# Kernel optimization log

Measured on AMD Instinct MI355X. Metric: run time of the kernel, lower is better.

The kernel has to match this reference:

```python
import jax, jax.numpy as jnp
import numpy as np

B, SEQ, ST, DIN, DK, DV = 2, 4096, 128, 1024, 64, 64
T = SEQ + 2 * ST  # 4352, divisible by 8 -> no pad branch in original


def _l2norm(t):
    # matches torch F.normalize(p=2, dim=-1, eps=1e-12)
    return t / jnp.maximum(jnp.linalg.norm(t, axis=-1, keepdims=True), 1e-12)


def setup_inputs() -> dict:
    key = jax.random.key(0)
    ks = jax.random.split(key, 9)
    x = jax.random.normal(ks[0], (B, T, DIN), dtype=jnp.float32)
    w = 0.02
    Wq = jax.random.normal(ks[1], (DK, DIN), dtype=jnp.float32) * w
    Wk = jax.random.normal(ks[2], (DK, DIN), dtype=jnp.float32) * w
    Wv = jax.random.normal(ks[3], (DV, DIN), dtype=jnp.float32) * w
    Wq_s = jax.random.normal(ks[4], (DK, DIN), dtype=jnp.float32) * w
    Wk_s = jax.random.normal(ks[5], (DK, DIN), dtype=jnp.float32) * w
    Wv_s = jax.random.normal(ks[6], (DV, DIN), dtype=jnp.float32) * w
    cope_emb = jax.random.normal(ks[7], (DK, T), dtype=jnp.float32)  # (1, dim_key, seq_len+2*state_len) squeezed
    scale = jnp.array([0.125], dtype=jnp.float32)  # learnable scaling_factor param
    return {"x": x, "Wq": Wq, "Wk": Wk, "Wv": Wv, "Wq_s": Wq_s,
            "Wk_s": Wk_s, "Wv_s": Wv_s, "cope_emb": cope_emb, "scale": scale}


def reference(x, Wq, Wk, Wv, Wq_s, Wk_s, Wv_s, cope_emb, scale):
    # extract_state: start-state, sequence, end-state
    xs, xm, xe = x[:, :ST], x[:, ST:ST + SEQ], x[:, ST + SEQ:]
    # project (Linear, no bias) then L2-normalize each token vector
    q = jnp.concatenate([_l2norm(xs @ Wq_s.T), _l2norm(xm @ Wq.T), _l2norm(xe @ Wq_s.T)], axis=1)
    k = jnp.concatenate([_l2norm(xs @ Wk_s.T), _l2norm(xm @ Wk.T), _l2norm(xe @ Wk_s.T)], axis=1)
    v = jnp.concatenate([_l2norm(xs @ Wv_s.T), _l2norm(xm @ Wv.T), _l2norm(xe @ Wv_s.T)], axis=1)

    # q@k^T is used both for CoPE gates and (scaled) attention scores
    logits = jnp.einsum('btd,bsd->bts', q, k)  # (B, T, T)

    # --- CoPE bias ---
    gates = jax.nn.sigmoid(logits)
    pos = jnp.cumsum(gates[:, :, ::-1], axis=-1)[:, :, ::-1]  # flip-cumsum-flip
    pos = jnp.minimum(pos, jnp.float32(T - 1))
    pos_floor = jnp.floor(pos)
    pos_ceil = jnp.ceil(pos)
    w = pos - pos_floor
    logits_int = jnp.einsum('btd,dl->btl', q, cope_emb)  # (B, T, T)
    lc = jnp.take_along_axis(logits_int, pos_ceil.astype(jnp.int32), axis=-1)
    lf = jnp.take_along_axis(logits_int, pos_floor.astype(jnp.int32), axis=-1)
    cope_bias = lc * w + lf * (1.0 - w)

    # --- causal + state-token mask: tril, with end-state rows blocked from start-state cols ---
    i = jnp.arange(T)
    mask = i[:, None] >= i[None, :]
    blocked = (i[:, None] >= SEQ + ST) & (i[None, :] < ST)
    mask = mask & (~blocked)
    attn_bias = jnp.where(mask, 0.0, -jnp.inf)[None, :, :]

    scores = logits * scale[0] + attn_bias + cope_bias
    att = jax.nn.softmax(scores, axis=-1) @ v  # (B, T, DV)
    return att
```

## Files before the change

### kernel.cpp

```cpp
#include <hip/hip_runtime.h>
#include <math.h>

#define B_ 2
#define SEQ_ 4096
#define ST_ 128
#define T_ 4352
#define DIN_ 1024
#define NW 16
#define LMAX 3328
#define LPAD 3336
#define NSLICE 272
#define NROW 8704

typedef _Float16 f16;
typedef __attribute__((ext_vector_type(8))) _Float16 f16x8;
typedef __attribute__((ext_vector_type(4))) float f32x4;

#define OB_WH  0
#define OB_WL  786432
#define OB_QH  1572864
#define OB_QL  2686976
#define OB_KH  3801088
#define OB_KL  4915200
#define OB_VT  6029312
#define OB_CPT 7143424
#define OB_SS  7569408
#define OB_XH  17039360
#define OB_XL  34865152
#define NEED_NEW 52690944ull

#define WT4_OFF 0
#define Q_OFF   393216
#define KT_OFF  950272
#define V_OFF   1507328

__device__ __forceinline__ int wuid() {
  return __builtin_amdgcn_readfirstlane((int)(threadIdx.x >> 6));
}

template<int CTRL, int RM>
__device__ __forceinline__ float dppadd(float x) {
  int y = __builtin_amdgcn_update_dpp(0, __float_as_int(x), CTRL, RM, 0xf, true);
  return x + __int_as_float(y);
}
__device__ __forceinline__ float wave_iscan(float x) {
  x = dppadd<0x111, 0xf>(x);
  x = dppadd<0x112, 0xf>(x);
  x = dppadd<0x114, 0xf>(x);
  x = dppadd<0x118, 0xf>(x);
  x = dppadd<0x142, 0xa>(x);
  x = dppadd<0x143, 0xc>(x);
  return x;
}
__device__ __forceinline__ float p16scan(float x) {
  x = dppadd<0x111, 0xf>(x);
  x = dppadd<0x112, 0xf>(x);
  x = dppadd<0x114, 0xf>(x);
  x = dppadd<0x118, 0xf>(x);
  return x;
}
__device__ __forceinline__ float swz15(float x) {
  return __int_as_float(__builtin_amdgcn_ds_swizzle(__float_as_int(x), 0x1F0));
}

__global__ __launch_bounds__(256) void wsplit_kernel(
    const float* __restrict__ Wq,  const float* __restrict__ Wk,
    const float* __restrict__ Wv,  const float* __restrict__ Wqs,
    const float* __restrict__ Wks, const float* __restrict__ Wvs,
    f16* __restrict__ wh, f16* __restrict__ wl) {
  const int m = blockIdx.y;
  const float* src = (m==0)?Wq:(m==1)?Wqs:(m==2)?Wk:(m==3)?Wks:(m==4)?Wv:Wvs;
  const int g0 = (int)blockIdx.x * 4096 + (int)threadIdx.x * 16;
  const float4* s4 = reinterpret_cast<const float4*>(src + g0);
  float4 v0 = s4[0], v1 = s4[1], v2 = s4[2], v3 = s4[3];
  f16x8 h0, h1, l0, l1;
  h0[0]=(f16)v0.x; h0[1]=(f16)v0.y; h0[2]=(f16)v0.z; h0[3]=(f16)v0.w;
  h0[4]=(f16)v1.x; h0[5]=(f16)v1.y; h0[6]=(f16)v1.z; h0[7]=(f16)v1.w;
  h1[0]=(f16)v2.x; h1[1]=(f16)v2.y; h1[2]=(f16)v2.z; h1[3]=(f16)v2.w;
  h1[4]=(f16)v3.x; h1[5]=(f16)v3.y; h1[6]=(f16)v3.z; h1[7]=(f16)v3.w;
  l0[0]=(f16)(v0.x-(float)h0[0]); l0[1]=(f16)(v0.y-(float)h0[1]);
  l0[2]=(f16)(v0.z-(float)h0[2]); l0[3]=(f16)(v0.w-(float)h0[3]);
  l0[4]=(f16)(v1.x-(float)h0[4]); l0[5]=(f16)(v1.y-(float)h0[5]);
  l0[6]=(f16)(v1.z-(float)h0[6]); l0[7]=(f16)(v1.w-(float)h0[7]);
  l1[0]=(f16)(v2.x-(float)h1[0]); l1[1]=(f16)(v2.y-(float)h1[1]);
  l1[2]=(f16)(v2.z-(float)h1[2]); l1[3]=(f16)(v2.w-(float)h1[3]);
  l1[4]=(f16)(v3.x-(float)h1[4]); l1[5]=(f16)(v3.y-(float)h1[5]);
  l1[6]=(f16)(v3.z-(float)h1[6]); l1[7]=(f16)(v3.w-(float)h1[7]);
  const size_t o = (size_t)m * 65536 + g0;
  *reinterpret_cast<f16x8*>(wh + o) = h0;
  *reinterpret_cast<f16x8*>(wh + o + 8) = h1;
  *reinterpret_cast<f16x8*>(wl + o) = l0;
  *reinterpret_cast<f16x8*>(wl + o + 8) = l1;
}

__global__ __launch_bounds__(256) void xsplit_kernel(
    const float* __restrict__ x, f16* __restrict__ xh, f16* __restrict__ xl) {
  const size_t g0 = ((size_t)blockIdx.x * 256 + threadIdx.x) * 16;
  const float4* s4 = reinterpret_cast<const float4*>(x + g0);
  float4 v0 = s4[0], v1 = s4[1], v2 = s4[2], v3 = s4[3];
  f16x8 h0, h1, l0, l1;
  h0[0]=(f16)v0.x; h0[1]=(f16)v0.y; h0[2]=(f16)v0.z; h0[3]=(f16)v0.w;
  h0[4]=(f16)v1.x; h0[5]=(f16)v1.y; h0[6]=(f16)v1.z; h0[7]=(f16)v1.w;
  h1[0]=(f16)v2.x; h1[1]=(f16)v2.y; h1[2]=(f16)v2.z; h1[3]=(f16)v2.w;
  h1[4]=(f16)v3.x; h1[5]=(f16)v3.y; h1[6]=(f16)v3.z; h1[7]=(f16)v3.w;
  l0[0]=(f16)(v0.x-(float)h0[0]); l0[1]=(f16)(v0.y-(float)h0[1]);
  l0[2]=(f16)(v0.z-(float)h0[2]); l0[3]=(f16)(v0.w-(float)h0[3]);
  l0[4]=(f16)(v1.x-(float)h0[4]); l0[5]=(f16)(v1.y-(float)h0[5]);
  l0[6]=(f16)(v1.z-(float)h0[6]); l0[7]=(f16)(v1.w-(float)h0[7]);
  l1[0]=(f16)(v2.x-(float)h1[0]); l1[1]=(f16)(v2.y-(float)h1[1]);
  l1[2]=(f16)(v2.z-(float)h1[2]); l1[3]=(f16)(v2.w-(float)h1[3]);
  l1[4]=(f16)(v3.x-(float)h1[4]); l1[5]=(f16)(v3.y-(float)h1[5]);
  l1[6]=(f16)(v3.z-(float)h1[6]); l1[7]=(f16)(v3.w-(float)h1[7]);
  *reinterpret_cast<f16x8*>(xh + g0) = h0;
  *reinterpret_cast<f16x8*>(xh + g0 + 8) = h1;
  *reinterpret_cast<f16x8*>(xl + g0) = l0;
  *reinterpret_cast<f16x8*>(xl + g0 + 8) = l1;
}

__global__ __launch_bounds__(256) void copet_kernel(
    const float* __restrict__ cope, f16* __restrict__ copeT) {
  __shared__ float t2[64][65];
  const int l0 = blockIdx.x << 6;
  const int tid = (int)threadIdx.x;
  #pragma unroll
  for (int p = 0; p < 16; ++p) {
    int d = (p << 2) + (tid >> 6), c = tid & 63;
    t2[d][c] = cope[(size_t)d * T_ + l0 + c];
  }
  __syncthreads();
  #pragma unroll
  for (int p = 0; p < 16; ++p) {
    int l = (p << 2) + (tid >> 6), d = tid & 63;
    copeT[(size_t)(l0 + l) * 64 + d] = (f16)t2[d][l];
  }
}

#define PM_MFMA(ACC, WHP, WLP) { \
  f16x8 bh_ = *reinterpret_cast<const f16x8*>((WHP) + (st << 5)); \
  f16x8 bl_ = *reinterpret_cast<const f16x8*>((WLP) + (st << 5)); \
  ACC = __builtin_amdgcn_mfma_f32_16x16x32_f16(xh_, bh_, ACC, 0, 0, 0); \
  ACC = __builtin_amdgcn_mfma_f32_16x16x32_f16(xl_, bh_, ACC, 0, 0, 0); \
  ACC = __builtin_amdgcn_mfma_f32_16x16x32_f16(xh_, bl_, ACC, 0, 0, 0); }

#define PM_RED(ACC, P) { \
  float s0_ = ACC[0]*ACC[0], s1_ = ACC[1]*ACC[1], s2_ = ACC[2]*ACC[2], s3_ = ACC[3]*ACC[3]; \
  s0_ += __shfl_xor(s0_, 1, 64); s1_ += __shfl_xor(s1_, 1, 64); \
  s2_ += __shfl_xor(s2_, 1, 64); s3_ += __shfl_xor(s3_, 1, 64); \
  s0_ += __shfl_xor(s0_, 2, 64); s1_ += __shfl_xor(s1_, 2, 64); \
  s2_ += __shfl_xor(s2_, 2, 64); s3_ += __shfl_xor(s3_, 2, 64); \
  s0_ += __shfl_xor(s0_, 4, 64); s1_ += __shfl_xor(s1_, 4, 64); \
  s2_ += __shfl_xor(s2_, 4, 64); s3_ += __shfl_xor(s3_, 4, 64); \
  s0_ += __shfl_xor(s0_, 8, 64); s1_ += __shfl_xor(s1_, 8, 64); \
  s2_ += __shfl_xor(s2_, 8, 64); s3_ += __shfl_xor(s3_, 8, 64); \
  if (qlo == 0) { \
    ssq[wn][P][(qhi << 2) + 0] = s0_; ssq[wn][P][(qhi << 2) + 1] = s1_; \
    ssq[wn][P][(qhi << 2) + 2] = s2_; ssq[wn][P][(qhi << 2) + 3] = s3_; } }

#define PM_QK1(ACC, P, HH, LL, RG) { \
  float tt_ = ssq[0][P][(qhi << 2) + RG] + ssq[1][P][(qhi << 2) + RG] \
            + ssq[2][P][(qhi << 2) + RG] + ssq[3][P][(qhi << 2) + RG]; \
  float rn_ = 1.f / fmaxf(sqrtf(tt_), 1e-12f); \
  float v_ = ACC[RG] * rn_; \
  f16 h_ = (f16)v_; \
  size_t ad_ = (size_t)(bt0 + (qhi << 2) + RG) * 64 + (wn << 4) + qlo; \
  HH[ad_] = h_; LL[ad_] = (f16)(v_ - (float)h_); }

#define PM_V1(ACC, P, RG) { \
  float tt_ = ssq[0][P][(qhi << 2) + RG] + ssq[1][P][(qhi << 2) + RG] \
            + ssq[2][P][(qhi << 2) + RG] + ssq[3][P][(qhi << 2) + RG]; \
  float rn_ = 1.f / fmaxf(sqrtf(tt_), 1e-12f); \
  vt[(size_t)(b * 64 + (wn << 4) + qlo) * T_ + t0 + (qhi << 2) + RG] = (f16)(ACC[RG] * rn_); }

__global__ __launch_bounds__(512, 4) void projM_kernel(
    const f16* __restrict__ xh, const f16* __restrict__ xl,
    const f16* __restrict__ wh, const f16* __restrict__ wl,
    f16* __restrict__ qh, f16* __restrict__ ql,
    f16* __restrict__ kh, f16* __restrict__ kl,
    f16* __restrict__ vt) {
  __shared__ float ssq[4][3][16];
  __shared__ float part[4][64][12];
  const int lane = (int)threadIdx.x & 63;
  const int w = wuid();
  const int wn = w & 3;
  const int kh2 = w >> 2;
  const int qlo = lane & 15, qhi = lane >> 4;
  const int bt0 = (int)blockIdx.x << 4;
  const int b = bt0 / T_;
  const int t0 = bt0 - b * T_;
  const int spec = (t0 < ST_ || t0 >= ST_ + SEQ_) ? 1 : 0;

  const int kof = kh2 << 9;
  const f16* xhr = xh + (size_t)(bt0 + qlo) * DIN_ + kof + (qhi << 3);
  const f16* xlr = xl + (size_t)(bt0 + qlo) * DIN_ + kof + (qhi << 3);
  const size_t wrow = (size_t)((wn << 4) + qlo) * 1024 + kof + (qhi << 3);
  const f16* wq  = wh + (size_t)(0 + spec) * 65536 + wrow;
  const f16* wqL = wl + (size_t)(0 + spec) * 65536 + wrow;
  const f16* wk  = wh + (size_t)(2 + spec) * 65536 + wrow;
  const f16* wkL = wl + (size_t)(2 + spec) * 65536 + wrow;
  const f16* wv  = wh + (size_t)(4 + spec) * 65536 + wrow;
  const f16* wvL = wl + (size_t)(4 + spec) * 65536 + wrow;

  f32x4 aq = {0.f,0.f,0.f,0.f}, ak = {0.f,0.f,0.f,0.f}, av = {0.f,0.f,0.f,0.f};

  #pragma unroll 4
  for (int st = 0; st < 16; ++st) {
    f16x8 xh_ = *reinterpret_cast<const f16x8*>(xhr + (st << 5));
    f16x8 xl_ = *reinterpret_cast<const f16x8*>(xlr + (st << 5));
    PM_MFMA(aq, wq, wqL)
    PM_MFMA(ak, wk, wkL)
    PM_MFMA(av, wv, wvL)
  }

  if (w >= 4) {
    float* p = &part[w - 4][lane][0];
    p[0] = aq[0]; p[1] = aq[1]; p[2]  = aq[2]; p[3]  = aq[3];
    p[4] = ak[0]; p[5] = ak[1]; p[6]  = ak[2]; p[7]  = ak[3];
    p[8] = av[0]; p[9] = av[1]; p[10] = av[2]; p[11] = av[3];
  }
  __syncthreads();
  if (w < 4) {
    const float* p = &part[w][lane][0];
    aq[0] += p[0]; aq[1] += p[1]; aq[2] += p[2];  aq[3] += p[3];
    ak[0] += p[4]; ak[1] += p[5]; ak[2] += p[6];  ak[3] += p[7];
    av[0] += p[8]; av[1] += p[9]; av[2] += p[10]; av[3] += p[11];
    PM_RED(aq, 0) PM_RED(ak, 1) PM_RED(av, 2)
  }
  __syncthreads();
  if (w < 4) {
    PM_QK1(aq, 0, qh, ql, 0) PM_QK1(aq, 0, qh, ql, 1)
    PM_QK1(aq, 0, qh, ql, 2) PM_QK1(aq, 0, qh, ql, 3)
    PM_QK1(ak, 1, kh, kl, 0) PM_QK1(ak, 1, kh, kl, 1)
    PM_QK1(ak, 1, kh, kl, 2) PM_QK1(ak, 1, kh, kl, 3)
    PM_V1(av, 2, 0) PM_V1(av, 2, 1) PM_V1(av, 2, 2) PM_V1(av, 2, 3)
  }
}

__global__ __launch_bounds__(512, 4) void gscan_kernel(
    const f16* __restrict__ qh, const f16* __restrict__ kh,
    float* __restrict__ ss) {
  __shared__ float sl[16][NSLICE];
  const int lane = (int)threadIdx.x & 63;
  const int w = wuid();
  const int qlo = lane & 15, qhi = lane >> 4;
  const int rowg0 = (int)blockIdx.x << 4;
  const int b = rowg0 / T_;
  const size_t bT64 = (size_t)(b * T_) * 64;
  const f16* qrp = qh + (size_t)(rowg0 + qlo) * 64 + (qhi << 3);
  f16x8 aqh0 = *reinterpret_cast<const f16x8*>(qrp);
  f16x8 aqh1 = *reinterpret_cast<const f16x8*>(qrp + 32);

  for (int i = 0; i < 34; ++i) {
    const int sli = w * 34 + i;
    const int sg = (sli << 4) + qlo;
    const f16* krh_ = kh + bT64 + (size_t)sg * 64 + (qhi << 3);
    f16x8 bh0 = *reinterpret_cast<const f16x8*>(krh_);
    f16x8 bh1 = *reinterpret_cast<const f16x8*>(krh_ + 32);
    f32x4 a = {0.f, 0.f, 0.f, 0.f};
    a = __builtin_amdgcn_mfma_f32_16x16x32_f16(aqh0, bh0, a, 0, 0, 0);
    a = __builtin_amdgcn_mfma_f32_16x16x32_f16(aqh1, bh1, a, 0, 0, 0);
    float g0 = 1.f / (1.f + __expf(-a[0])); float s0 = p16scan(g0);
    float g1 = 1.f / (1.f + __expf(-a[1])); float s1 = p16scan(g1);
    float g2 = 1.f / (1.f + __expf(-a[2])); float s2 = p16scan(g2);
    float g3 = 1.f / (1.f + __expf(-a[3])); float s3 = p16scan(g3);
    if (qlo == 15) {
      sl[(qhi << 2) + 0][sli] = s0;
      sl[(qhi << 2) + 1][sli] = s1;
      sl[(qhi << 2) + 2][sli] = s2;
      sl[(qhi << 2) + 3][sli] = s3;
    }
  }
  __syncthreads();
  #pragma unroll
  for (int rr = 0; rr < 2; ++rr) {
    const int row = (w << 1) | rr;
    const float* r = &sl[row][0];
    const int base = NSLICE - 1 - 5 * lane;
    double v0 = 0.0, v1 = 0.0, v2 = 0.0, v3 = 0.0, v4 = 0.0;
    double acc = 0.0;
    if (base - 0 >= 0) { acc += (double)r[base - 0]; } v0 = acc;
    if (base - 1 >= 0) { acc += (double)r[base - 1]; } v1 = acc;
    if (base - 2 >= 0) { acc += (double)r[base - 2]; } v2 = acc;
    if (base - 3 >= 0) { acc += (double)r[base - 3]; } v3 = acc;
    if (base - 4 >= 0) { acc += (double)r[base - 4]; } v4 = acc;
    double x = acc;
    #pragma unroll
    for (int off = 1; off < 64; off <<= 1) {
      double y = __shfl_up(x, off, 64);
      if (lane >= off) x += y;
    }
    const double offn = x - acc;
    float* go = ss + (size_t)(rowg0 + row) * NSLICE;
    if (base - 0 >= 0) go[base - 0] = (float)(v0 + offn);
    if (base - 1 >= 0) go[base - 1] = (float)(v1 + offn);
    if (base - 2 >= 0) go[base - 2] = (float)(v2 + offn);
    if (base - 3 >= 0) go[base - 3] = (float)(v3 + offn);
    if (base - 4 >= 0) go[base - 4] = (float)(v4 + offn);
  }
}

#define QKD(SF, NF) { \
  int sg_ = swb + (NF << 4) + qlo; \
  int scl_ = sg_ < T_ ? sg_ : T_ - 1; \
  const f16* krh_ = kh + bT64 + (size_t)scl_ * 64 + (qhi << 3); \
  f16x8 bh0_ = *reinterpret_cast<const f16x8*>(krh_); \
  f16x8 bh1_ = *reinterpret_cast<const f16x8*>(krh_ + 32); \
  f32x4 a_ = {0.f, 0.f, 0.f, 0.f}; \
  a_ = __builtin_amdgcn_mfma_f32_16x16x32_f16(aqh0, bh0_, a_, 0, 0, 0); \
  a_ = __builtin_amdgcn_mfma_f32_16x16x32_f16(aqh1, bh1_, a_, 0, 0, 0); \
  SF = a_; }

#define PXA(SF, RG, SSV, LF, LC, WF) { \
  float g_ = 1.f / (1.f + __expf(-SF[RG])); \
  float in_ = p16scan(g_); \
  float pos_ = SSV - in_ + g_; \
  pos_ = pos_ < 0.f ? 0.f : (pos_ > 3326.f ? 3326.f : pos_); \
  int idx_ = (int)pos_; \
  WF = pos_ - (float)idx_; \
  const f16* lrow_ = liL + ((qhi << 2) + RG) * LPAD + idx_; \
  LF = (float)lrow_[0]; LC = (float)lrow_[1]; }

#define PXB(SF, NF, RG, LF, LC, WF) { \
  int sg_ = swb + (NF << 4) + qlo; \
  float bias_ = fmaf(WF, LC - LF, LF); \
  int tl_ = t0 + (qhi << 2) + RG; \
  bool valid_ = (sg_ <= tl_) && !((tl_ >= ST_ + SEQ_) && (sg_ < ST_)); \
  float p_ = valid_ ? __expf(fmaf(SF[RG], sc, bias_) - mrw[RG]) : 0.f; \
  lsum[RG] += p_; \
  pst[((qhi << 2) + RG) * 40 + (NF << 4) + qlo] = (f16)p_; }

#define PVF(OA, NF) { \
  int d_ = (NF << 4) + qlo; \
  const f16* vr_ = vt + (size_t)(b * 64 + d_) * T_; \
  f16x8 v0_ = *reinterpret_cast<const f16x8*>(vr_ + sv0); \
  OA = __builtin_amdgcn_mfma_f32_16x16x32_f16(pa0, v0_, OA, 0, 0, 0); }

#define OST(OA, NF) { \
  ob[w * 1024 + ((qhi << 2) + 0) * 64 + (NF << 4) + qlo] = OA[0]; \
  ob[w * 1024 + ((qhi << 2) + 1) * 64 + (NF << 4) + qlo] = OA[1]; \
  ob[w * 1024 + ((qhi << 2) + 2) * 64 + (NF << 4) + qlo] = OA[2]; \
  ob[w * 1024 + ((qhi << 2) + 3) * 64 + (NF << 4) + qlo] = OA[3]; }

__global__ __launch_bounds__(1024, 4) void attnD_kernel(
    const f16* __restrict__ qh, const f16* __restrict__ kh,
    const f16* __restrict__ vt, const f16* __restrict__ cpt,
    const float* __restrict__ ss,
    const float* __restrict__ scalep, float* __restrict__ out) {
  __shared__ __align__(16) f16 liL[16 * LPAD];
  __shared__ __align__(16) f16 pstage[NW * 16 * 40];
  __shared__ float totF[NW][16];
  __shared__ float rmxS[NW][16];

  const int tid = (int)threadIdx.x;
  const int lane = tid & 63;
  const int w = wuid();
  const int bt0 = ((int)(gridDim.x - 1 - blockIdx.x)) << 4;
  const int b = bt0 / T_;
  const int t0 = bt0 - b * T_;
  const float sc = scalep[0];
  const int qlo = lane & 15, qhi = lane >> 4;

  const f16* qrp = qh + (size_t)(bt0 + qlo) * 64 + (qhi << 3);
  f16x8 aqh0 = *reinterpret_cast<const f16x8*>(qrp);
  f16x8 aqh1 = *reinterpret_cast<const f16x8*>(qrp + 32);

  {
    f32x4 rm = {-1e30f, -1e30f, -1e30f, -1e30f};
    #pragma unroll 2
    for (int c = 0; c < 13; ++c) {
      const int lf = w * 208 + (c << 4);
      const f16* cr = cpt + (size_t)(lf + qlo) * 64 + (qhi << 3);
      f16x8 b0 = *reinterpret_cast<const f16x8*>(cr);
      f16x8 b1 = *reinterpret_cast<const f16x8*>(cr + 32);
      f32x4 a = {0.f, 0.f, 0.f, 0.f};
      a = __builtin_amdgcn_mfma_f32_16x16x32_f16(aqh0, b0, a, 0, 0, 0);
      a = __builtin_amdgcn_mfma_f32_16x16x32_f16(aqh1, b1, a, 0, 0, 0);
      f16 h0_ = (f16)a[0]; liL[((qhi << 2) + 0) * LPAD + lf + qlo] = h0_; rm[0] = fmaxf(rm[0], (float)h0_);
      f16 h1_ = (f16)a[1]; liL[((qhi << 2) + 1) * LPAD + lf + qlo] = h1_; rm[1] = fmaxf(rm[1], (float)h1_);
      f16 h2_ = (f16)a[2]; liL[((qhi << 2) + 2) * LPAD + lf + qlo] = h2_; rm[2] = fmaxf(rm[2], (float)h2_);
      f16 h3_ = (f16)a[3]; liL[((qhi << 2) + 3) * LPAD + lf + qlo] = h3_; rm[3] = fmaxf(rm[3], (float)h3_);
    }
    #pragma unroll
    for (int k = 1; k < 16; k <<= 1) {
      rm[0] = fmaxf(rm[0], __shfl_xor(rm[0], k, 64));
      rm[1] = fmaxf(rm[1], __shfl_xor(rm[1], k, 64));
      rm[2] = fmaxf(rm[2], __shfl_xor(rm[2], k, 64));
      rm[3] = fmaxf(rm[3], __shfl_xor(rm[3], k, 64));
    }
    if (qlo == 0) {
      rmxS[w][(qhi << 2) + 0] = rm[0];
      rmxS[w][(qhi << 2) + 1] = rm[1];
      rmxS[w][(qhi << 2) + 2] = rm[2];
      rmxS[w][(qhi << 2) + 3] = rm[3];
    }
  }
  __syncthreads();
  f32x4 mrw;
  #pragma unroll
  for (int reg = 0; reg < 4; ++reg) {
    float mm = rmxS[0][(qhi << 2) + reg];
    #pragma unroll
    for (int w2 = 1; w2 < NW; ++w2) mm = fmaxf(mm, rmxS[w2][(qhi << 2) + reg]);
    mrw[reg] = mm + fabsf(sc) + 2e-3f;
  }

  f16* pst = pstage + w * 640;
  const size_t bT64 = (size_t)(b * T_) * 64;
  const float* ssl = ss + (size_t)(bt0 + (qhi << 2)) * NSLICE;

  f32x4 o0 = {0.f,0.f,0.f,0.f}, o1 = {0.f,0.f,0.f,0.f};
  f32x4 o2 = {0.f,0.f,0.f,0.f}, o3 = {0.f,0.f,0.f,0.f};
  f32x4 lsum = {0.f,0.f,0.f,0.f};

  const int jtmax = (t0 + 15) >> 9;
  for (int jt = jtmax; jt >= 0; --jt) {
    const int swb = (jt << 9) + (w << 5);
    f32x4 sf0, sf1;
    QKD(sf0, 0) QKD(sf1, 1)
    const int sbr = swb >> 4;
    const int sb0 = sbr < (NSLICE - 1) ? sbr : (NSLICE - 1);
    const int sb1 = (sbr + 1) < (NSLICE - 1) ? (sbr + 1) : (NSLICE - 1);
    float sA0 = ssl[0 * NSLICE + sb0];
    float sA1 = ssl[1 * NSLICE + sb0];
    float sA2 = ssl[2 * NSLICE + sb0];
    float sA3 = ssl[3 * NSLICE + sb0];
    float sB0 = ssl[0 * NSLICE + sb1];
    float sB1 = ssl[1 * NSLICE + sb1];
    float sB2 = ssl[2 * NSLICE + sb1];
    float sB3 = ssl[3 * NSLICE + sb1];
    float lf0, lc0, wf0, lf1, lc1, wf1, lf2, lc2, wf2, lf3, lc3, wf3;
    float lf4, lc4, wf4, lf5, lc5, wf5, lf6, lc6, wf6, lf7, lc7, wf7;
    PXA(sf0, 0, sA0, lf0, lc0, wf0) PXA(sf0, 1, sA1, lf1, lc1, wf1)
    PXA(sf0, 2, sA2, lf2, lc2, wf2) PXA(sf0, 3, sA3, lf3, lc3, wf3)
    PXA(sf1, 0, sB0, lf4, lc4, wf4) PXA(sf1, 1, sB1, lf5, lc5, wf5)
    PXA(sf1, 2, sB2, lf6, lc6, wf6) PXA(sf1, 3, sB3, lf7, lc7, wf7)
    PXB(sf0, 0, 0, lf0, lc0, wf0) PXB(sf0, 0, 1, lf1, lc1, wf1)
    PXB(sf0, 0, 2, lf2, lc2, wf2) PXB(sf0, 0, 3, lf3, lc3, wf3)
    PXB(sf1, 1, 0, lf4, lc4, wf4) PXB(sf1, 1, 1, lf5, lc5, wf5)
    PXB(sf1, 1, 2, lf6, lc6, wf6) PXB(sf1, 1, 3, lf7, lc7, wf7)
    {
      const f16* pr = pst + qlo * 40;
      f16x8 pa0 = *reinterpret_cast<const f16x8*>(pr + (qhi << 3));
      int sv0 = swb + (qhi << 3);
      sv0 = sv0 < T_ - 8 ? sv0 : T_ - 8;
      PVF(o0, 0) PVF(o1, 1) PVF(o2, 2) PVF(o3, 3)
    }
  }

  #pragma unroll
  for (int k = 1; k < 16; k <<= 1) {
    lsum[0] += __shfl_xor(lsum[0], k, 64);
    lsum[1] += __shfl_xor(lsum[1], k, 64);
    lsum[2] += __shfl_xor(lsum[2], k, 64);
    lsum[3] += __shfl_xor(lsum[3], k, 64);
  }
  __syncthreads();
  if (qlo == 0) {
    totF[w][(qhi << 2) + 0] = lsum[0];
    totF[w][(qhi << 2) + 1] = lsum[1];
    totF[w][(qhi << 2) + 2] = lsum[2];
    totF[w][(qhi << 2) + 3] = lsum[3];
  }
  float* ob = reinterpret_cast<float*>(liL);
  OST(o0, 0) OST(o1, 1) OST(o2, 2) OST(o3, 3)
  __syncthreads();
  {
    const int r = tid >> 6, d = tid & 63;
    float L = 0.f, o = 0.f;
    #pragma unroll
    for (int w2 = 0; w2 < NW; ++w2) {
      L += totF[w2][r];
      o += ob[w2 * 1024 + tid];
    }
    out[(size_t)(bt0 + r) * 64 + d] = o / L;
  }
}

__global__ __launch_bounds__(256) void wtrans_kernel(
    const float* __restrict__ Wq,  const float* __restrict__ Wk,
    const float* __restrict__ Wv,  const float* __restrict__ Wqs,
    const float* __restrict__ Wks, const float* __restrict__ Wvs,
    float* __restrict__ ws) {
  const int m = blockIdx.y;
  const float* src = (m==0)?Wq:(m==1)?Wqs:(m==2)?Wk:(m==3)?Wks:(m==4)?Wv:Wvs;
  float* dst = ws + (size_t)m * (DIN_*64);
  const int bx = blockIdx.x;
  #pragma unroll
  for (int p = 0; p < 16; ++p) {
    int e = (int)threadIdx.x + (p << 8);
    int c = e & 3, o = (e >> 2) & 63;
    int i = (bx << 6) + (p << 2) + c;
    dst[(((bx << 4) + p) * 64 + o) * 4 + c] = src[o * DIN_ + i];
  }
}

__global__ __launch_bounds__(256) void proj_kernel(
    const float* __restrict__ x, float* __restrict__ ws) {
  __shared__ float tile[32][65];
  const int t0 = blockIdx.x << 5;
  const int b  = blockIdx.y;
  const int pj = blockIdx.z;
  const int spec = (t0 < ST_ || t0 >= ST_ + SEQ_) ? 1 : 0;
  const float4* W4 = reinterpret_cast<const float4*>(ws + WT4_OFF + (size_t)(pj*2 + spec) * (DIN_*64));
  const int lane = (int)threadIdx.x & 63;
  const int w = wuid();
  const float* xb = x + ((size_t)(b * T_ + t0 + (w << 3))) * DIN_;
  float acc[8] = {0.f,0.f,0.f,0.f,0.f,0.f,0.f,0.f};
  #pragma unroll 4
  for (int i4 = 0; i4 < 256; ++i4) {
    float4 wv = W4[(i4 << 6) + lane];
    #pragma unroll
    for (int r = 0; r < 8; ++r) {
      float4 xv = reinterpret_cast<const float4*>(xb + r * DIN_)[i4];
      acc[r] = fmaf(wv.x, xv.x, fmaf(wv.y, xv.y, fmaf(wv.z, xv.z, fmaf(wv.w, xv.w, acc[r]))));
    }
  }
  float outv[8];
  #pragma unroll
  for (int r = 0; r < 8; ++r) {
    float sq = acc[r] * acc[r];
    #pragma unroll
    for (int off = 32; off; off >>= 1) sq += __shfl_xor(sq, off, 64);
    float n = fmaxf(sqrtf(sq), 1e-12f);
    outv[r] = acc[r] / n;
  }
  const int trow = t0 + (w << 3);
  if (pj != 1) {
    float* dst = ws + (pj == 0 ? Q_OFF : V_OFF) + ((size_t)(b * T_ + trow)) * 64;
    #pragma unroll
    for (int r = 0; r < 8; ++r) dst[r * 64 + lane] = outv[r];
  } else {
    #pragma unroll
    for (int r = 0; r < 8; ++r) tile[(w << 3) + r][lane] = outv[r];
    __syncthreads();
    float* kt = ws + KT_OFF + (size_t)b * 16 * T_ * 4;
    #pragma unroll
    for (int p = 0; p < 8; ++p) {
      int e = (int)threadIdx.x + (p << 8);
      int c = e & 3, tt = (e >> 2) & 31, d4 = e >> 7;
      kt[((size_t)d4 * T_ + t0 + tt) * 4 + c] = tile[tt][(d4 << 2) + c];
    }
  }
}

__global__ __launch_bounds__(1024) void attn_kernel(
    const float* __restrict__ ws_c, const float* __restrict__ cope,
    const float* __restrict__ scalep, float* __restrict__ out) {
  __shared__ float li_s[8 * T_];
  __shared__ float pbuf[NW][8][32];
  __shared__ float totF[NW][8];
  __shared__ double suffD[NW][8];
  __shared__ double carryD[2][8];
  __shared__ float mlL[NW][8];
  __shared__ float wmax[NW][8];
  const int tid = (int)threadIdx.x;
  const int lane = tid & 63;
  const int w = wuid();
  const int t0 = ((int)(gridDim.x - 1 - blockIdx.x)) << 3;
  const int b  = blockIdx.y;
  const float* qrow = ws_c + Q_OFF + ((size_t)(b * T_ + t0)) * 64;
  const float* ktb  = ws_c + KT_OFF + (size_t)b * 16 * T_ * 4;
  const float* vb   = ws_c + V_OFF + ((size_t)b * T_) * 64;
  const float sc = scalep[0];
  if (tid < 8) carryD[0][tid] = 0.0;
  float lm[8];
  #pragma unroll
  for (int r = 0; r < 8; ++r) lm[r] = -INFINITY;
  for (int jt = 0; jt < 5; ++jt) {
    const int l = (jt << 10) + tid;
    if (l < T_) {
      float a[8] = {0,0,0,0,0,0,0,0};
      #pragma unroll 4
      for (int d4 = 0; d4 < 16; ++d4) {
        float c0 = cope[(d4 * 4 + 0) * T_ + l];
        float c1 = cope[(d4 * 4 + 1) * T_ + l];
        float c2 = cope[(d4 * 4 + 2) * T_ + l];
        float c3 = cope[(d4 * 4 + 3) * T_ + l];
        #pragma unroll
        for (int r = 0; r < 8; ++r) {
          float4 qq = *reinterpret_cast<const float4*>(qrow + r * 64 + (d4 << 2));
          a[r] = fmaf(c0, qq.x, fmaf(c1, qq.y, fmaf(c2, qq.z, fmaf(c3, qq.w, a[r]))));
        }
      }
      #pragma unroll
      for (int r = 0; r < 8; ++r) { li_s[r * T_ + l] = a[r]; lm[r] = fmaxf(lm[r], a[r]); }
    }
  }
  #pragma unroll
  for (int r = 0; r < 8; ++r) {
    #pragma unroll
    for (int off = 32; off; off >>= 1) lm[r] = fmaxf(lm[r], __shfl_xor(lm[r], off, 64));
  }
  if (lane == 0) {
    #pragma unroll
    for (int r = 0; r < 8; ++r) wmax[w][r] = lm[r];
  }
  __syncthreads();
  float mrow[8];
  #pragma unroll
  for (int r = 0; r < 8; ++r) {
    float mm = wmax[0][r];
    #pragma unroll
    for (int w2 = 1; w2 < NW; ++w2) mm = fmaxf(mm, wmax[w2][r]);
    mrow[r] = mm + fabsf(sc) + 1e-3f;
  }
  float acc[8]  = {0,0,0,0,0,0,0,0};
  float lsum[8] = {0,0,0,0,0,0,0,0};
  int par = 0;
  for (int jt = 4; jt >= 0; --jt) {
    const int s = (jt << 10) + tid;
    const bool sval = (s < T_);
    float lg[8] = {0,0,0,0,0,0,0,0};
    if (sval) {
      #pragma unroll 4
      for (int d4 = 0; d4 < 16; ++d4) {
        float4 kk = *reinterpret_cast<const float4*>(ktb + ((size_t)d4 * T_ + s) * 4);
        #pragma unroll
        for (int r = 0; r < 8; ++r) {
          float4 qq = *reinterpret_cast<const float4*>(qrow + r * 64 + (d4 << 2));
          lg[r] = fmaf(kk.x, qq.x, fmaf(kk.y, qq.y, fmaf(kk.z, qq.z, fmaf(kk.w, qq.w, lg[r]))));
        }
      }
    }
    float locsuf[8], gtot[8];
    #pragma unroll
    for (int r = 0; r < 8; ++r) {
      float g = sval ? 1.f / (1.f + __expf(-lg[r])) : 0.f;
      float xx = wave_iscan(g);
      float tt = __shfl(xx, 63, 64);
      locsuf[r] = tt - xx + g;
      gtot[r] = tt;
    }
    if (lane == 0) {
      #pragma unroll
      for (int r = 0; r < 8; ++r) totF[w][r] = gtot[r];
    }
    __syncthreads();
    if (tid < 128) {
      const int w2 = tid >> 3, r = tid & 7;
      float ssum = 0.f;
      for (int w3 = w2 + 1; w3 < NW; ++w3) ssum += totF[w3][r];
      suffD[w2][r] = carryD[par][r] + (double)ssum;
      if (w2 == 0) carryD[par ^ 1][r] = carryD[par][r] + (double)(ssum + totF[0][r]);
    }
    __syncthreads();
    par ^= 1;
    if ((jt << 10) > t0 + 7) continue;
    float p[8];
    #pragma unroll
    for (int r = 0; r < 8; ++r) {
      double posd = suffD[w][r] + (double)locsuf[r];
      if (posd > 4351.0) posd = 4351.0;
      int idx = (int)posd;
      float wf = (float)(posd - (double)idx);
      int idx2 = idx < 4351 ? idx + 1 : 4351;
      float lf = li_s[r * T_ + idx];
      float lc = li_s[r * T_ + idx2];
      float bias = fmaf(wf, lc - lf, lf);
      const int t = t0 + r;
      const bool valid = sval && (s <= t) && !((t >= ST_ + SEQ_) && (s < ST_));
      float score = valid ? fmaf(lg[r], sc, bias) : -INFINITY;
      p[r] = __expf(score - mrow[r]);
      lsum[r] += p[r];
    }
    const int sbase = (jt << 10) + (w << 6);
    if (sbase < T_) {
      #pragma unroll
      for (int pass = 0; pass < 2; ++pass) {
        if ((lane >> 5) == pass) {
          #pragma unroll
          for (int r = 0; r < 8; ++r) pbuf[w][r][lane & 31] = p[r];
        }
        const int s0 = sbase + (pass << 5);
        #pragma unroll 4
        for (int s4 = 0; s4 < 8; ++s4) {
          const int sb = s0 + (s4 << 2);
          float v0 = vb[(size_t)(sb + 0) * 64 + lane];
          float v1 = vb[(size_t)(sb + 1) * 64 + lane];
          float v2 = vb[(size_t)(sb + 2) * 64 + lane];
          float v3 = vb[(size_t)(sb + 3) * 64 + lane];
          #pragma unroll
          for (int r = 0; r < 8; ++r) {
            float4 pr = *reinterpret_cast<const float4*>(&pbuf[w][r][s4 << 2]);
            acc[r] = fmaf(pr.x, v0, fmaf(pr.y, v1, fmaf(pr.z, v2, fmaf(pr.w, v3, acc[r]))));
          }
        }
      }
    }
  }
  #pragma unroll
  for (int r = 0; r < 8; ++r) {
    #pragma unroll
    for (int off = 32; off; off >>= 1) lsum[r] += __shfl_xor(lsum[r], off, 64);
  }
  if (lane == 0) {
    #pragma unroll
    for (int r = 0; r < 8; ++r) mlL[w][r] = lsum[r];
  }
  float* pb = &pbuf[w][0][0];
  #pragma unroll
  for (int pass = 0; pass < 2; ++pass) {
    __syncthreads();
    #pragma unroll
    for (int rr = 0; rr < 4; ++rr) pb[rr * 64 + lane] = acc[pass * 4 + rr];
    __syncthreads();
    if (tid < 256) {
      const int rr = tid >> 6, d = tid & 63;
      const int r = pass * 4 + rr;
      float o = 0.f, L = 0.f;
      #pragma unroll
      for (int w2 = 0; w2 < NW; ++w2) {
        o += (&pbuf[w2][0][0])[rr * 64 + d];
        L += mlL[w2][r];
      }
      out[((size_t)(b * T_ + t0 + r)) * 64 + d] = o / L;
    }
  }
}

extern "C" void kernel_launch(void* const* d_in, const int* in_sizes, int n_in,
                              void* d_out, int out_size, void* d_ws, size_t ws_size,
                              hipStream_t stream) {
  const float* x    = (const float*)d_in[0];
  const float* Wq   = (const float*)d_in[1];
  const float* Wk   = (const float*)d_in[2];
  const float* Wv   = (const float*)d_in[3];
  const float* Wqs  = (const float*)d_in[4];
  const float* Wks  = (const float*)d_in[5];
  const float* Wvs  = (const float*)d_in[6];
  const float* cope = (const float*)d_in[7];
  const float* scl  = (const float*)d_in[8];
  float* outp = (float*)d_out;
  (void)in_sizes; (void)n_in; (void)out_size;

  if (ws_size >= NEED_NEW) {
    unsigned char* wb = (unsigned char*)d_ws;
    f16* whp = (f16*)(wb + OB_WH);
    f16* wlp = (f16*)(wb + OB_WL);
    f16* qh = (f16*)(wb + OB_QH);
    f16* ql = (f16*)(wb + OB_QL);
    f16* kh = (f16*)(wb + OB_KH);
    f16* kl = (f16*)(wb + OB_KL);
    f16* vt = (f16*)(wb + OB_VT);
    f16* cpt = (f16*)(wb + OB_CPT);
    float* ssp = (float*)(wb + OB_SS);
    f16* xhp = (f16*)(wb + OB_XH);
    f16* xlp = (f16*)(wb + OB_XL);
    hipLaunchKernelGGL(wsplit_kernel, dim3(16, 6), dim3(256), 0, stream,
                       Wq, Wk, Wv, Wqs, Wks, Wvs, whp, wlp);
    hipLaunchKernelGGL(xsplit_kernel, dim3(2176), dim3(256), 0, stream, x, xhp, xlp);
    hipLaunchKernelGGL(copet_kernel, dim3(52), dim3(256), 0, stream, cope, cpt);
    hipLaunchKernelGGL(projM_kernel, dim3(544), dim3(512), 0, stream,
                       xhp, xlp, whp, wlp, qh, ql, kh, kl, vt);
    hipLaunchKernelGGL(gscan_kernel, dim3(544), dim3(512), 0, stream, qh, kh, ssp);
    hipLaunchKernelGGL(attnD_kernel, dim3(544), dim3(1024), 0, stream,
                       qh, kh, vt, cpt, ssp, scl, outp);
  } else {
    float* ws = (float*)d_ws;
    hipLaunchKernelGGL(wtrans_kernel, dim3(16, 6), dim3(256), 0, stream,
                       Wq, Wk, Wv, Wqs, Wks, Wvs, ws);
    hipLaunchKernelGGL(proj_kernel, dim3(136, 2, 3), dim3(256), 0, stream, x, ws);
    hipLaunchKernelGGL(attn_kernel, dim3(544, 2), dim3(1024), 0, stream, ws, cope, scl, outp);
  }
}
```

Baseline: 251.9 us.

## Fuse gate suffix-scan kernel into attention kernel via shared-memory slice sums

Merges the separate gscan kernel into the attention kernel. Each block now computes the per-slice sigmoid-gate sums and their reverse prefix scan itself, keeps them in shared memory, and reads them from there instead of from a global buffer. This removes a kernel launch and the global write and read of the slice-sum array. In exchange each attention block does the full-row QK gate scan inline, adding shared memory and work to a kernel that is already heavy, which may reduce occupancy.

After: 250.5 us. About the same (-0.5%).

```diff
diff --git a/kernel.cpp b/kernel.cpp
--- a/kernel.cpp
+++ b/kernel.cpp
@@ -235,22 +235,105 @@
   }
 }
 
-__global__ __launch_bounds__(512, 4) void gscan_kernel(
+#define QKD(SF, NF) { \
+  int sg_ = swb + (NF << 4) + qlo; \
+  int scl_ = sg_ < T_ ? sg_ : T_ - 1; \
+  const f16* krh_ = kh + bT64 + (size_t)scl_ * 64 + (qhi << 3); \
+  f16x8 bh0_ = *reinterpret_cast<const f16x8*>(krh_); \
+  f16x8 bh1_ = *reinterpret_cast<const f16x8*>(krh_ + 32); \
+  f32x4 a_ = {0.f, 0.f, 0.f, 0.f}; \
+  a_ = __builtin_amdgcn_mfma_f32_16x16x32_f16(aqh0, bh0_, a_, 0, 0, 0); \
+  a_ = __builtin_amdgcn_mfma_f32_16x16x32_f16(aqh1, bh1_, a_, 0, 0, 0); \
+  SF = a_; }
+
+#define PXA(SF, RG, SSV, LF, LC, WF) { \
+  float g_ = 1.f / (1.f + __expf(-SF[RG])); \
+  float in_ = p16scan(g_); \
+  float pos_ = SSV - in_ + g_; \
+  pos_ = pos_ < 0.f ? 0.f : (pos_ > 3326.f ? 3326.f : pos_); \
+  int idx_ = (int)pos_; \
+  WF = pos_ - (float)idx_; \
+  const f16* lrow_ = liL + ((qhi << 2) + RG) * LPAD + idx_; \
+  LF = (float)lrow_[0]; LC = (float)lrow_[1]; }
+
+#define PXB(SF, NF, RG, LF, LC, WF) { \
+  int sg_ = swb + (NF << 4) + qlo; \
+  float bias_ = fmaf(WF, LC - LF, LF); \
+  int tl_ = t0 + (qhi << 2) + RG; \
+  bool valid_ = (sg_ <= tl_) && !((tl_ >= ST_ + SEQ_) && (sg_ < ST_)); \
+  float p_ = valid_ ? __expf(fmaf(SF[RG], sc, bias_) - mrw[RG]) : 0.f; \
+  lsum[RG] += p_; \
+  pst[((qhi << 2) + RG) * 40 + (NF << 4) + qlo] = (f16)p_; }
+
+#define PVF(OA, NF) { \
+  int d_ = (NF << 4) + qlo; \
+  const f16* vr_ = vt + (size_t)(b * 64 + d_) * T_; \
+  f16x8 v0_ = *reinterpret_cast<const f16x8*>(vr_ + sv0); \
+  OA = __builtin_amdgcn_mfma_f32_16x16x32_f16(pa0, v0_, OA, 0, 0, 0); }
+
+#define OST(OA, NF) { \
+  ob[w * 1024 + ((qhi << 2) + 0) * 64 + (NF << 4) + qlo] = OA[0]; \
+  ob[w * 1024 + ((qhi << 2) + 1) * 64 + (NF << 4) + qlo] = OA[1]; \
+  ob[w * 1024 + ((qhi << 2) + 2) * 64 + (NF << 4) + qlo] = OA[2]; \
+  ob[w * 1024 + ((qhi << 2) + 3) * 64 + (NF << 4) + qlo] = OA[3]; }
+
+__global__ __launch_bounds__(1024, 4) void attnE_kernel(
     const f16* __restrict__ qh, const f16* __restrict__ kh,
-    float* __restrict__ ss) {
+    const f16* __restrict__ vt, const f16* __restrict__ cpt,
+    const float* __restrict__ scalep, float* __restrict__ out) {
+  __shared__ __align__(16) f16 liL[16 * LPAD];
+  __shared__ __align__(16) f16 pstage[NW * 16 * 40];
   __shared__ float sl[16][NSLICE];
-  const int lane = (int)threadIdx.x & 63;
+  __shared__ float totF[NW][16];
+  __shared__ float rmxS[NW][16];
+
+  const int tid = (int)threadIdx.x;
+  const int lane = tid & 63;
   const int w = wuid();
+  const int bt0 = ((int)(gridDim.x - 1 - blockIdx.x)) << 4;
+  const int b = bt0 / T_;
+  const int t0 = bt0 - b * T_;
+  const float sc = scalep[0];
   const int qlo = lane & 15, qhi = lane >> 4;
-  const int rowg0 = (int)blockIdx.x << 4;
-  const int b = rowg0 / T_;
-  const size_t bT64 = (size_t)(b * T_) * 64;
-  const f16* qrp = qh + (size_t)(rowg0 + qlo) * 64 + (qhi << 3);
+
+  const f16* qrp = qh + (size_t)(bt0 + qlo) * 64 + (qhi << 3);
   f16x8 aqh0 = *reinterpret_cast<const f16x8*>(qrp);
   f16x8 aqh1 = *reinterpret_cast<const f16x8*>(qrp + 32);
-
-  for (int i = 0; i < 34; ++i) {
-    const int sli = w * 34 + i;
+  const size_t bT64 = (size_t)(b * T_) * 64;
+
+  {
+    f32x4 rm = {-1e30f, -1e30f, -1e30f, -1e30f};
+    #pragma unroll 2
+    for (int c = 0; c < 13; ++c) {
+      const int lf = w * 208 + (c << 4);
+      const f16* cr = cpt + (size_t)(lf + qlo) * 64 + (qhi << 3);
+      f16x8 b0 = *reinterpret_cast<const f16x8*>(cr);
+      f16x8 b1 = *reinterpret_cast<const f16x8*>(cr + 32);
+      f32x4 a = {0.f, 0.f, 0.f, 0.f};
+      a = __builtin_amdgcn_mfma_f32_16x16x32_f16(aqh0, b0, a, 0, 0, 0);
+      a = __builtin_amdgcn_mfma_f32_16x16x32_f16(aqh1, b1, a, 0, 0, 0);
+      f16 h0_ = (f16)a[0]; liL[((qhi << 2) + 0) * LPAD + lf + qlo] = h0_; rm[0] = fmaxf(rm[0], (float)h0_);
+      f16 h1_ = (f16)a[1]; liL[((qhi << 2) + 1) * LPAD + lf + qlo] = h1_; rm[1] = fmaxf(rm[1], (float)h1_);
+      f16 h2_ = (f16)a[2]; liL[((qhi << 2) + 2) * LPAD + lf + qlo] = h2_; rm[2] = fmaxf(rm[2], (float)h2_);
+      f16 h3_ = (f16)a[3]; liL[((qhi << 2) + 3) * LPAD + lf + qlo] = h3_; rm[3] = fmaxf(rm[3], (float)h3_);
+    }
+    #pragma unroll
+    for (int k = 1; k < 16; k <<= 1) {
+      rm[0] = fmaxf(rm[0], __shfl_xor(rm[0], k, 64));
+      rm[1] = fmaxf(rm[1], __shfl_xor(rm[1], k, 64));
+      rm[2] = fmaxf(rm[2], __shfl_xor(rm[2], k, 64));
+      rm[3] = fmaxf(rm[3], __shfl_xor(rm[3], k, 64));
+    }
+    if (qlo == 0) {
+      rmxS[w][(qhi << 2) + 0] = rm[0];
+      rmxS[w][(qhi << 2) + 1] = rm[1];
+      rmxS[w][(qhi << 2) + 2] = rm[2];
+      rmxS[w][(qhi << 2) + 3] = rm[3];
+    }
+  }
+
+  for (int i = 0; i < 17; ++i) {
+    const int sli = w * 17 + i;
     const int sg = (sli << 4) + qlo;
     const f16* krh_ = kh + bT64 + (size_t)sg * 64 + (qhi << 3);
     f16x8 bh0 = *reinterpret_cast<const f16x8*>(krh_);
@@ -270,10 +353,10 @@
     }
   }
   __syncthreads();
-  #pragma unroll
-  for (int rr = 0; rr < 2; ++rr) {
-    const int row = (w << 1) | rr;
-    const float* r = &sl[row][0];
+
+  {
+    const int row = w;
+    float* r = &sl[row][0];
     const int base = NSLICE - 1 - 5 * lane;
     double v0 = 0.0, v1 = 0.0, v2 = 0.0, v3 = 0.0, v4 = 0.0;
     double acc = 0.0;
@@ -289,111 +372,13 @@
       if (lane >= off) x += y;
     }
     const double offn = x - acc;
-    float* go = ss + (size_t)(rowg0 + row) * NSLICE;
-    if (base - 0 >= 0) go[base - 0] = (float)(v0 + offn);
-    if (base - 1 >= 0) go[base - 1] = (float)(v1 + offn);
-    if (base - 2 >= 0) go[base - 2] = (float)(v2 + offn);
-    if (base - 3 >= 0) go[base - 3] = (float)(v3 + offn);
-    if (base - 4 >= 0) go[base - 4] = (float)(v4 + offn);
-  }
-}
-
-#define QKD(SF, NF) { \
-  int sg_ = swb + (NF << 4) + qlo; \
-  int scl_ = sg_ < T_ ? sg_ : T_ - 1; \
-  const f16* krh_ = kh + bT64 + (size_t)scl_ * 64 + (qhi << 3); \
-  f16x8 bh0_ = *reinterpret_cast<const f16x8*>(krh_); \
-  f16x8 bh1_ = *reinterpret_cast<const f16x8*>(krh_ + 32); \
-  f32x4 a_ = {0.f, 0.f, 0.f, 0.f}; \
-  a_ = __builtin_amdgcn_mfma_f32_16x16x32_f16(aqh0, bh0_, a_, 0, 0, 0); \
-  a_ = __builtin_amdgcn_mfma_f32_16x16x32_f16(aqh1, bh1_, a_, 0, 0, 0); \
-  SF = a_; }
-
-#define PXA(SF, RG, SSV, LF, LC, WF) { \
-  float g_ = 1.f / (1.f + __expf(-SF[RG])); \
-  float in_ = p16scan(g_); \
-  float pos_ = SSV - in_ + g_; \
-  pos_ = pos_ < 0.f ? 0.f : (pos_ > 3326.f ? 3326.f : pos_); \
-  int idx_ = (int)pos_; \
-  WF = pos_ - (float)idx_; \
-  const f16* lrow_ = liL + ((qhi << 2) + RG) * LPAD + idx_; \
-  LF = (float)lrow_[0]; LC = (float)lrow_[1]; }
-
-#define PXB(SF, NF, RG, LF, LC, WF) { \
-  int sg_ = swb + (NF << 4) + qlo; \
-  float bias_ = fmaf(WF, LC - LF, LF); \
-  int tl_ = t0 + (qhi << 2) + RG; \
-  bool valid_ = (sg_ <= tl_) && !((tl_ >= ST_ + SEQ_) && (sg_ < ST_)); \
-  float p_ = valid_ ? __expf(fmaf(SF[RG], sc, bias_) - mrw[RG]) : 0.f; \
-  lsum[RG] += p_; \
-  pst[((qhi << 2) + RG) * 40 + (NF << 4) + qlo] = (f16)p_; }
-
-#define PVF(OA, NF) { \
-  int d_ = (NF << 4) + qlo; \
-  const f16* vr_ = vt + (size_t)(b * 64 + d_) * T_; \
-  f16x8 v0_ = *reinterpret_cast<const f16x8*>(vr_ + sv0); \
-  OA = __builtin_amdgcn_mfma_f32_16x16x32_f16(pa0, v0_, OA, 0, 0, 0); }
-
-#define OST(OA, NF) { \
-  ob[w * 1024 + ((qhi << 2) + 0) * 64 + (NF << 4) + qlo] = OA[0]; \
-  ob[w * 1024 + ((qhi << 2) + 1) * 64 + (NF << 4) + qlo] = OA[1]; \
-  ob[w * 1024 + ((qhi << 2) + 2) * 64 + (NF << 4) + qlo] = OA[2]; \
-  ob[w * 1024 + ((qhi << 2) + 3) * 64 + (NF << 4) + qlo] = OA[3]; }
-
-__global__ __launch_bounds__(1024, 4) void attnD_kernel(
-    const f16* __restrict__ qh, const f16* __restrict__ kh,
-    const f16* __restrict__ vt, const f16* __restrict__ cpt,
-    const float* __restrict__ ss,
-    const float* __restrict__ scalep, float* __restrict__ out) {
-  __shared__ __align__(16) f16 liL[16 * LPAD];
-  __shared__ __align__(16) f16 pstage[NW * 16 * 40];
-  __shared__ float totF[NW][16];
-  __shared__ float rmxS[NW][16];
-
-  const int tid = (int)threadIdx.x;
-  const int lane = tid & 63;
-  const int w = wuid();
-  const int bt0 = ((int)(gridDim.x - 1 - blockIdx.x)) << 4;
-  const int b = bt0 / T_;
-  const int t0 = bt0 - b * T_;
-  const float sc = scalep[0];
-  const int qlo = lane & 15, qhi = lane >> 4;
-
-  const f16* qrp = qh + (size_t)(bt0 + qlo) * 64 + (qhi << 3);
-  f16x8 aqh0 = *reinterpret_cast<const f16x8*>(qrp);
-  f16x8 aqh1 = *reinterpret_cast<const f16x8*>(qrp + 32);
-
-  {
-    f32x4 rm = {-1e30f, -1e30f, -1e30f, -1e30f};
-    #pragma unroll 2
-    for (int c = 0; c < 13; ++c) {
-      const int lf = w * 208 + (c << 4);
-      const f16* cr = cpt + (size_t)(lf + qlo) * 64 + (qhi << 3);
-      f16x8 b0 = *reinterpret_cast<const f16x8*>(cr);
-      f16x8 b1 = *reinterpret_cast<const f16x8*>(cr + 32);
-      f32x4 a = {0.f, 0.f, 0.f, 0.f};
-      a = __builtin_amdgcn_mfma_f32_16x16x32_f16(aqh0, b0, a, 0, 0, 0);
-      a = __builtin_amdgcn_mfma_f32_16x16x32_f16(aqh1, b1, a, 0, 0, 0);
-      f16 h0_ = (f16)a[0]; liL[((qhi << 2) + 0) * LPAD + lf + qlo] = h0_; rm[0] = fmaxf(rm[0], (float)h0_);
-      f16 h1_ = (f16)a[1]; liL[((qhi << 2) + 1) * LPAD + lf + qlo] = h1_; rm[1] = fmaxf(rm[1], (float)h1_);
-      f16 h2_ = (f16)a[2]; liL[((qhi << 2) + 2) * LPAD + lf + qlo] = h2_; rm[2] = fmaxf(rm[2], (float)h2_);
-      f16 h3_ = (f16)a[3]; liL[((qhi << 2) + 3) * LPAD + lf + qlo] = h3_; rm[3] = fmaxf(rm[3], (float)h3_);
-    }
-    #pragma unroll
-    for (int k = 1; k < 16; k <<= 1) {
-      rm[0] = fmaxf(rm[0], __shfl_xor(rm[0], k, 64));
-      rm[1] = fmaxf(rm[1], __shfl_xor(rm[1], k, 64));
-      rm[2] = fmaxf(rm[2], __shfl_xor(rm[2], k, 64));
-      rm[3] = fmaxf(rm[3], __shfl_xor(rm[3], k, 64));
-    }
-    if (qlo == 0) {
-      rmxS[w][(qhi << 2) + 0] = rm[0];
-      rmxS[w][(qhi << 2) + 1] = rm[1];
-      rmxS[w][(qhi << 2) + 2] = rm[2];
-      rmxS[w][(qhi << 2) + 3] = rm[3];
-    }
-  }
-  __syncthreads();
+    if (base - 0 >= 0) r[base - 0] = (float)(v0 + offn);
+    if (base - 1 >= 0) r[base - 1] = (float)(v1 + offn);
+    if (base - 2 >= 0) r[base - 2] = (float)(v2 + offn);
+    if (base - 3 >= 0) r[base - 3] = (float)(v3 + offn);
+    if (base - 4 >= 0) r[base - 4] = (float)(v4 + offn);
+  }
+
   f32x4 mrw;
   #pragma unroll
   for (int reg = 0; reg < 4; ++reg) {
@@ -402,10 +387,9 @@
     for (int w2 = 1; w2 < NW; ++w2) mm = fmaxf(mm, rmxS[w2][(qhi << 2) + reg]);
     mrw[reg] = mm + fabsf(sc) + 2e-3f;
   }
+  __syncthreads();
 
   f16* pst = pstage + w * 640;
-  const size_t bT64 = (size_t)(b * T_) * 64;
-  const float* ssl = ss + (size_t)(bt0 + (qhi << 2)) * NSLICE;
 
   f32x4 o0 = {0.f,0.f,0.f,0.f}, o1 = {0.f,0.f,0.f,0.f};
   f32x4 o2 = {0.f,0.f,0.f,0.f}, o3 = {0.f,0.f,0.f,0.f};
@@ -419,14 +403,14 @@
     const int sbr = swb >> 4;
     const int sb0 = sbr < (NSLICE - 1) ? sbr : (NSLICE - 1);
     const int sb1 = (sbr + 1) < (NSLICE - 1) ? (sbr + 1) : (NSLICE - 1);
-    float sA0 = ssl[0 * NSLICE + sb0];
-    float sA1 = ssl[1 * NSLICE + sb0];
-    float sA2 = ssl[2 * NSLICE + sb0];
-    float sA3 = ssl[3 * NSLICE + sb0];
-    float sB0 = ssl[0 * NSLICE + sb1];
-    float sB1 = ssl[1 * NSLICE + sb1];
-    float sB2 = ssl[2 * NSLICE + sb1];
-    float sB3 = ssl[3 * NSLICE + sb1];
+    float sA0 = sl[(qhi << 2) + 0][sb0];
+    float sA1 = sl[(qhi << 2) + 1][sb0];
+    float sA2 = sl[(qhi << 2) + 2][sb0];
+    float sA3 = sl[(qhi << 2) + 3][sb0];
+    float sB0 = sl[(qhi << 2) + 0][sb1];
+    float sB1 = sl[(qhi << 2) + 1][sb1];
+    float sB2 = sl[(qhi << 2) + 2][sb1];
+    float sB3 = sl[(qhi << 2) + 3][sb1];
     float lf0, lc0, wf0, lf1, lc1, wf1, lf2, lc2, wf2, lf3, lc3, wf3;
     float lf4, lc4, wf4, lf5, lc5, wf5, lf6, lc6, wf6, lf7, lc7, wf7;
     PXA(sf0, 0, sA0, lf0, lc0, wf0) PXA(sf0, 1, sA1, lf1, lc1, wf1)
@@ -742,7 +726,6 @@
     f16* kl = (f16*)(wb + OB_KL);
     f16* vt = (f16*)(wb + OB_VT);
     f16* cpt = (f16*)(wb + OB_CPT);
-    float* ssp = (float*)(wb + OB_SS);
     f16* xhp = (f16*)(wb + OB_XH);
     f16* xlp = (f16*)(wb + OB_XL);
     hipLaunchKernelGGL(wsplit_kernel, dim3(16, 6), dim3(256), 0, stream,
@@ -751,9 +734,8 @@
     hipLaunchKernelGGL(copet_kernel, dim3(52), dim3(256), 0, stream, cope, cpt);
     hipLaunchKernelGGL(projM_kernel, dim3(544), dim3(512), 0, stream,
                        xhp, xlp, whp, wlp, qh, ql, kh, kl, vt);
-    hipLaunchKernelGGL(gscan_kernel, dim3(544), dim3(512), 0, stream, qh, kh, ssp);
-    hipLaunchKernelGGL(attnD_kernel, dim3(544), dim3(1024), 0, stream,
-                       qh, kh, vt, cpt, ssp, scl, outp);
+    hipLaunchKernelGGL(attnE_kernel, dim3(544), dim3(1024), 0, stream,
+                       qh, kh, vt, cpt, scl, outp);
   } else {
     float* ws = (float*)d_ws;
     hipLaunchKernelGGL(wtrans_kernel, dim3(16, 6), dim3(256), 0, stream,
```
